# Optimization experiments

Hardware: AMD Instinct MI355X
Metric: run time of the kernel (lower is better)

Reference implementation:

```python
import jax, jax.numpy as jnp
import numpy as np
import math

ROPE_THETA = 10000.0


def apply_rope(x, positions):
    # x: [B, H, S, d_k], positions: [S]
    d_k = x.shape[-1]
    inv_freq = 1.0 / (ROPE_THETA ** (jnp.arange(0, d_k, 2, dtype=jnp.float32) / d_k))  # [d_k/2]
    angles = positions.astype(jnp.float32)[:, None] * inv_freq[None, :]  # [S, d_k/2]
    cos = jnp.cos(angles)
    sin = jnp.sin(angles)
    x1 = x[..., 0::2]
    x2 = x[..., 1::2]
    r1 = x1 * cos - x2 * sin
    r2 = x1 * sin + x2 * cos
    out = jnp.stack([r1, r2], axis=-1)  # interleave pairs back
    return out.reshape(x.shape)


def setup_inputs() -> dict:
    key = jax.random.key(0)
    k1, k2, k3 = jax.random.split(key, 3)
    B, S, D = 4, 2048, 1024
    x = jax.random.normal(k1, (B, S, D), dtype=jnp.float32)
    token_positions = jnp.arange(S, dtype=jnp.int32)
    w_qkv = jax.random.normal(k2, (3 * D, D), dtype=jnp.float32) * (1.0 / math.sqrt(D))
    w_o = jax.random.normal(k3, (D, D), dtype=jnp.float32) * (1.0 / math.sqrt(D))
    return {"x": x, "token_positions": token_positions, "w_qkv": w_qkv, "w_o": w_o}


def reference(x, token_positions, w_qkv, w_o):
    B, S, D = x.shape
    H = 16
    d_k = D // H
    qkv = jnp.einsum('bsd,ed->bse', x, w_qkv)  # [B, S, 3D]
    # rearrange '... s (stack h dk) -> stack ... h s dk'
    qkv = qkv.reshape(B, S, 3, H, d_k)
    q = jnp.transpose(qkv[:, :, 0], (0, 2, 1, 3))  # [B, H, S, dk]
    k = jnp.transpose(qkv[:, :, 1], (0, 2, 1, 3))
    v = jnp.transpose(qkv[:, :, 2], (0, 2, 1, 3))
    q = apply_rope(q, token_positions)
    k = apply_rope(k, token_positions)
    scores = jnp.einsum('bhqd,bhkd->bhqk', q, k) / math.sqrt(d_k)
    causal = jnp.tril(jnp.ones((S, S), dtype=bool))
    scores = jnp.where(causal[None, None], scores, -jnp.inf)
    attn = jax.nn.softmax(scores, axis=-1)
    out = jnp.einsum('bhqk,bhkd->bhqd', attn, v)  # [B, H, S, dk]
    out = jnp.transpose(out, (0, 2, 1, 3)).reshape(B, S, D)
    return jnp.einsum('bsd,ed->bse', out, w_o)
```

## Files before the change

kernel.cpp:

```cpp
#include <hip/hip_runtime.h>
#include <hip/hip_bf16.h>
#include <math.h>

typedef __bf16 bf16_t;
typedef __attribute__((ext_vector_type(8))) __bf16 bf16x8;
typedef __attribute__((ext_vector_type(4))) __bf16 bf16x4;
typedef __attribute__((ext_vector_type(4))) float f32x4;

#define MFMA_16x16x32(A_, B_, C_) __builtin_amdgcn_mfma_f32_16x16x32_bf16((A_), (B_), (C_), 0, 0, 0)

#define Bsz 4
#define Ssz 2048
#define Dsz 1024
#define Hh 16
#define DKd 64
#define Mrows (Bsz * Ssz)
#define N1 (3 * Dsz)
#define KD Dsz

__global__ void cvt_f32_bf16_kernel(const float* __restrict__ src, bf16_t* __restrict__ dst, int n4) {
  int i = blockIdx.x * blockDim.x + threadIdx.x;
  if (i >= n4) return;
  float4 v = reinterpret_cast<const float4*>(src)[i];
  bf16x4 o = {(bf16_t)v.x, (bf16_t)v.y, (bf16_t)v.z, (bf16_t)v.w};
  reinterpret_cast<bf16x4*>(dst)[i] = o;
}

__global__ void rope_tab_kernel(const int* __restrict__ pos, float2* __restrict__ tab) {
  int i = blockIdx.x * blockDim.x + threadIdx.x;
  if (i >= Ssz * 32) return;
  int s = i >> 5, f = i & 31;
  float inv_freq = powf(10000.0f, -(float)(2 * f) / 64.0f);
  float a = (float)pos[s] * inv_freq;
  tab[i] = make_float2(cosf(a), sinf(a));
}

template <int EPI>
__global__ __launch_bounds__(256, 3) void gemm_tn_kernel(
    const bf16_t* __restrict__ A, const bf16_t* __restrict__ Bt, int Kdim, int ldcN,
    bf16_t* __restrict__ qb, bf16_t* __restrict__ kb, bf16_t* __restrict__ vtb,
    const float2* __restrict__ tab, float* __restrict__ fout) {
  __shared__ __align__(16) bf16_t As[2][128 * 32];
  __shared__ __align__(16) bf16_t Bs[2][128 * 32];
  const int t = threadIdx.x;
  const int w = t >> 6, l = t & 63;
  const int lr = l & 15, lk = l >> 4;
  const int wm = w >> 1, wn = w & 1;
  const int m0 = blockIdx.y * 128, n0 = blockIdx.x * 128;

  const int srow = t >> 2;
  const int schunk = (t & 3) ^ ((t >> 3) & 3);
  const bf16_t* gA = A + (size_t)(m0 + srow) * Kdim + schunk * 8;
  const bf16_t* gB = Bt + (size_t)(n0 + srow) * Kdim + schunk * 8;

  f32x4 acc[4][4] = {};
  const int rsw = (lr >> 1) & 3;

#define STAGE_(PH, KT)                                                                   \
  do {                                                                                   \
    __builtin_amdgcn_global_load_lds(gA + (KT), &As[PH][(w * 16) * 32], 16, 0, 0);       \
    __builtin_amdgcn_global_load_lds(gA + (size_t)64 * Kdim + (KT),                      \
                                     &As[PH][(64 + w * 16) * 32], 16, 0, 0);             \
    __builtin_amdgcn_global_load_lds(gB + (KT), &Bs[PH][(w * 16) * 32], 16, 0, 0);       \
    __builtin_amdgcn_global_load_lds(gB + (size_t)64 * Kdim + (KT),                      \
                                     &Bs[PH][(64 + w * 16) * 32], 16, 0, 0);             \
  } while (0)

#define COMPUTE_(PH)                                                                     \
  do {                                                                                   \
    bf16x8 af[4], bfv[4];                                                                \
    _Pragma("unroll") for (int m = 0; m < 4; ++m) af[m] =                                \
        *reinterpret_cast<const bf16x8*>(&As[PH][(wm * 64 + m * 16 + lr) * 32] +         \
                                         ((lk ^ rsw) * 8));                              \
    _Pragma("unroll") for (int n = 0; n < 4; ++n) bfv[n] =                               \
        *reinterpret_cast<const bf16x8*>(&Bs[PH][(wn * 64 + n * 16 + lr) * 32] +         \
                                         ((lk ^ rsw) * 8));                              \
    _Pragma("unroll") for (int m = 0; m < 4; ++m) _Pragma("unroll") for (int n = 0;      \
                                                                         n < 4; ++n)    \
        acc[m][n] = MFMA_16x16x32(af[m], bfv[n], acc[m][n]);                             \
  } while (0)

  STAGE_(0, 0);
  __syncthreads();
  for (int kt = 0; kt < Kdim; kt += 64) {
    STAGE_(1, kt + 32);
    COMPUTE_(0);
    __syncthreads();
    if (kt + 64 < Kdim) STAGE_(0, kt + 64);
    COMPUTE_(1);
    __syncthreads();
  }
#undef STAGE_
#undef COMPUTE_

  if (EPI == 0) {
#pragma unroll
    for (int n = 0; n < 4; ++n) {
      const int col = n0 + wn * 64 + n * 16 + lr;
      const int sect = col >> 10;
      const int h = (col >> 6) & 15;
      const int dk = col & 63;
#pragma unroll
      for (int m = 0; m < 4; ++m) {
        const int growb = m0 + wm * 64 + m * 16 + lk * 4;
#pragma unroll
        for (int r = 0; r < 4; ++r) {
          const int grow = growb + r;
          const int bb = grow >> 11;
          const int s = grow & (Ssz - 1);
          float v = acc[m][n][r];
          if (sect < 2) {
            const float pv = __shfl_xor(v, 1);
            const float2 cs = tab[(s << 5) | (dk >> 1)];
            float vr = (dk & 1) ? (pv * cs.y + v * cs.x) : (v * cs.x - pv * cs.y);
            const size_t idx = ((size_t)((bb * Hh + h) * Ssz + s)) * DKd + dk;
            if (sect == 0)
              qb[idx] = (bf16_t)(vr * 0.125f);
            else
              kb[idx] = (bf16_t)vr;
          } else {
            vtb[((size_t)(bb * Hh + h) * DKd + dk) * Ssz + s] = (bf16_t)v;
          }
        }
      }
    }
  } else {
#pragma unroll
    for (int m = 0; m < 4; ++m)
#pragma unroll
      for (int r = 0; r < 4; ++r) {
        const int grow = m0 + wm * 64 + m * 16 + lk * 4 + r;
        float* op = fout + (size_t)grow * ldcN + n0 + wn * 64 + lr;
#pragma unroll
        for (int n = 0; n < 4; ++n) op[n * 16] = acc[m][n][r];
      }
  }
}

__global__ __launch_bounds__(256, 3) void attn_kernel(
    const bf16_t* __restrict__ qb, const bf16_t* __restrict__ kb,
    const bf16_t* __restrict__ vtb, bf16_t* __restrict__ aout) {
  __shared__ __align__(16) bf16_t Ks[64 * 64];
  __shared__ __align__(16) bf16_t Vs[64 * 64];
  const int t = threadIdx.x, w = t >> 6, l = t & 63;
  const int lr = l & 15, lk = l >> 4;
  const int bid = blockIdx.x;
  const int bh = (bid & 7) * 8 + ((bid >> 3) & 7);
  const int qt = 15 - (bid >> 6);
  const int q0 = qt * 128;
  const int sub0 = q0 + w * 32;

  const bf16_t* qbase = qb + ((size_t)bh * Ssz + sub0) * DKd;
  bf16x8 qf[2][2];
#pragma unroll
  for (int s = 0; s < 2; ++s) {
    qf[s][0] = *reinterpret_cast<const bf16x8*>(qbase + (s * 16 + lr) * DKd + lk * 8);
    qf[s][1] = *reinterpret_cast<const bf16x8*>(qbase + (s * 16 + lr) * DKd + 32 + lk * 8);
  }

  f32x4 o[2][4] = {};
  float mrow[2] = {-INFINITY, -INFINITY};
  float lsum[2] = {0.f, 0.f};

  const int srow = t >> 2;
  const int scc = (t & 3) * 2;
  const bf16_t* kg = kb + ((size_t)bh * Ssz + srow) * DKd + scc * 8;
  const bf16_t* vg = vtb + ((size_t)bh * DKd + srow) * Ssz + scc * 8;
  bf16_t* ksw0 = Ks + srow * 64 + ((scc ^ (srow & 7)) * 8);
  bf16_t* ksw1 = Ks + srow * 64 + (((scc + 1) ^ (srow & 7)) * 8);
  bf16_t* vw[4];
#pragma unroll
  for (int u = 0; u < 2; ++u) {
    const int c = scc + u;
    const int B = 32 * (c >> 2) + 16 * (c & 1) + 4 * ((c & 3) >> 1);
    const int ch = B >> 3, off = B & 7;
    vw[2 * u] = Vs + srow * 64 + ((ch ^ (srow & 7)) * 8) + off;
    vw[2 * u + 1] = Vs + srow * 64 + (((ch + 1) ^ (srow & 7)) * 8) + off;
  }

  const int kvend = q0 + 128;
  bf16x8 pk0 = *reinterpret_cast<const bf16x8*>(kg);
  bf16x8 pk1 = *reinterpret_cast<const bf16x8*>(kg + 8);
  bf16x8 pv0 = *reinterpret_cast<const bf16x8*>(vg);
  bf16x8 pv1 = *reinterpret_cast<const bf16x8*>(vg + 8);

  for (int kv = 0; kv < kvend; kv += 64) {
    __syncthreads();
    *reinterpret_cast<bf16x8*>(ksw0) = pk0;
    *reinterpret_cast<bf16x8*>(ksw1) = pk1;
    *reinterpret_cast<bf16x4*>(vw[0]) = __builtin_shufflevector(pv0, pv0, 0, 1, 2, 3);
    *reinterpret_cast<bf16x4*>(vw[1]) = __builtin_shufflevector(pv0, pv0, 4, 5, 6, 7);
    *reinterpret_cast<bf16x4*>(vw[2]) = __builtin_shufflevector(pv1, pv1, 0, 1, 2, 3);
    *reinterpret_cast<bf16x4*>(vw[3]) = __builtin_shufflevector(pv1, pv1, 4, 5, 6, 7);
    __syncthreads();
    if (kv + 64 < kvend) {
      pk0 = *reinterpret_cast<const bf16x8*>(kg + (size_t)(kv + 64) * DKd);
      pk1 = *reinterpret_cast<const bf16x8*>(kg + (size_t)(kv + 64) * DKd + 8);
      pv0 = *reinterpret_cast<const bf16x8*>(vg + kv + 64);
      pv1 = *reinterpret_cast<const bf16x8*>(vg + kv + 64 + 8);
    }
#pragma unroll
    for (int s = 0; s < 2; ++s) {
      const int subrow = sub0 + s * 16;
      if (kv > subrow + 15) continue;
      f32x4 sa[4];
#pragma unroll
      for (int n = 0; n < 4; ++n) {
        const int R = n * 16 + lr;
        const bf16x8 a0 = *reinterpret_cast<const bf16x8*>(Ks + R * 64 + ((lk ^ (R & 7)) * 8));
        const bf16x8 a1 = *reinterpret_cast<const bf16x8*>(Ks + R * 64 + (((lk + 4) ^ (R & 7)) * 8));
        f32x4 z = {};
        z = MFMA_16x16x32(a0, qf[s][0], z);
        z = MFMA_16x16x32(a1, qf[s][1], z);
        sa[n] = z;
      }
      if (kv + 63 > subrow) {
        const int qrow = subrow + lr;
        const int kbase = kv + lk * 4;
#pragma unroll
        for (int n = 0; n < 4; ++n)
#pragma unroll
          for (int r = 0; r < 4; ++r)
            if (kbase + n * 16 + r > qrow) sa[n][r] = -INFINITY;
      }
      float mx = fmaxf(fmaxf(fmaxf(sa[0][0], sa[0][1]), fmaxf(sa[0][2], sa[0][3])),
                       fmaxf(fmaxf(sa[1][0], sa[1][1]), fmaxf(sa[1][2], sa[1][3])));
      mx = fmaxf(mx, fmaxf(fmaxf(fmaxf(sa[2][0], sa[2][1]), fmaxf(sa[2][2], sa[2][3])),
                           fmaxf(fmaxf(sa[3][0], sa[3][1]), fmaxf(sa[3][2], sa[3][3]))));
      mx = fmaxf(mx, __shfl_xor(mx, 16));
      mx = fmaxf(mx, __shfl_xor(mx, 32));
      const float mnew = fmaxf(mrow[s], mx);
      const float scl = __expf(mrow[s] - mnew);
      mrow[s] = mnew;
      float ps = 0.f;
#pragma unroll
      for (int n = 0; n < 4; ++n)
#pragma unroll
        for (int r = 0; r < 4; ++r) {
          const float p = __expf(sa[n][r] - mnew);
          sa[n][r] = p;
          ps += p;
        }
      lsum[s] = lsum[s] * scl + ps;
#pragma unroll
      for (int n = 0; n < 4; ++n)
#pragma unroll
        for (int r = 0; r < 4; ++r) o[s][n][r] *= scl;
      bf16x8 pb0, pb1;
#pragma unroll
      for (int r = 0; r < 4; ++r) {
        pb0[r] = (bf16_t)sa[0][r];
        pb0[4 + r] = (bf16_t)sa[1][r];
        pb1[r] = (bf16_t)sa[2][r];
        pb1[4 + r] = (bf16_t)sa[3][r];
      }
#pragma unroll
      for (int n = 0; n < 4; ++n) {
        const int R = n * 16 + lr;
        const bf16x8 v0 = *reinterpret_cast<const bf16x8*>(Vs + R * 64 + ((lk ^ (R & 7)) * 8));
        const bf16x8 v1 = *reinterpret_cast<const bf16x8*>(Vs + R * 64 + (((lk + 4) ^ (R & 7)) * 8));
        o[s][n] = MFMA_16x16x32(v0, pb0, o[s][n]);
        o[s][n] = MFMA_16x16x32(v1, pb1, o[s][n]);
      }
    }
  }
  const int b_ = bh >> 4, h_ = bh & 15;
#pragma unroll
  for (int s = 0; s < 2; ++s) {
    float sm = lsum[s];
    sm += __shfl_xor(sm, 16);
    sm += __shfl_xor(sm, 32);
    const float inv = 1.0f / sm;
    const int qrow = sub0 + s * 16 + lr;
    bf16_t* op = aout + ((size_t)b_ * Ssz + qrow) * Dsz + h_ * DKd + lk * 4;
#pragma unroll
    for (int n = 0; n < 4; ++n) {
      const bf16x4 ov = {(bf16_t)(o[s][n][0] * inv), (bf16_t)(o[s][n][1] * inv),
                         (bf16_t)(o[s][n][2] * inv), (bf16_t)(o[s][n][3] * inv)};
      *reinterpret_cast<bf16x4*>(op + n * 16) = ov;
    }
  }
}

extern "C" void kernel_launch(void* const* d_in, const int* in_sizes, int n_in,
                              void* d_out, int out_size, void* d_ws, size_t ws_size,
                              hipStream_t stream) {
  const float* x = (const float*)d_in[0];
  const int* pos = (const int*)d_in[1];
  const float* wqkv = (const float*)d_in[2];
  const float* wo = (const float*)d_in[3];
  float* out = (float*)d_out;

  bf16_t* xb = (bf16_t*)d_ws;
  bf16_t* wqkvb = xb + (size_t)Mrows * KD;
  bf16_t* wob = wqkvb + (size_t)N1 * KD;
  bf16_t* qbuf = wob + (size_t)Dsz * KD;
  bf16_t* kbuf = qbuf + (size_t)64 * Ssz * DKd;
  bf16_t* vtb = kbuf + (size_t)64 * Ssz * DKd;
  float2* tab = (float2*)(vtb + (size_t)64 * Ssz * DKd);
  bf16_t* aout = xb;

  {
    int n4 = Mrows * KD / 4;
    cvt_f32_bf16_kernel<<<(n4 + 255) / 256, 256, 0, stream>>>(x, xb, n4);
  }
  {
    int n4 = N1 * KD / 4;
    cvt_f32_bf16_kernel<<<(n4 + 255) / 256, 256, 0, stream>>>(wqkv, wqkvb, n4);
  }
  {
    int n4 = Dsz * KD / 4;
    cvt_f32_bf16_kernel<<<(n4 + 255) / 256, 256, 0, stream>>>(wo, wob, n4);
  }
  rope_tab_kernel<<<(Ssz * 32 + 255) / 256, 256, 0, stream>>>(pos, tab);

  gemm_tn_kernel<0><<<dim3(N1 / 128, Mrows / 128), 256, 0, stream>>>(
      xb, wqkvb, KD, 0, qbuf, kbuf, vtb, tab, nullptr);

  attn_kernel<<<dim3(16 * 64), 256, 0, stream>>>(qbuf, kbuf, vtb, aout);

  gemm_tn_kernel<1><<<dim3(Dsz / 128, Mrows / 128), 256, 0, stream>>>(
      aout, wob, KD, Dsz, nullptr, nullptr, nullptr, nullptr, out);
}
```

Baseline: 217.8 us.

## Add 256x256-tile QKV GEMM with direct global-to-LDS loads

```diff
diff --git a/kernel.cpp b/kernel.cpp
--- a/kernel.cpp
+++ b/kernel.cpp
@@ -35,11 +35,119 @@
   tab[i] = make_float2(cosf(a), sinf(a));
 }
 
-template <int EPI>
-__global__ __launch_bounds__(256, 3) void gemm_tn_kernel(
+__global__ __launch_bounds__(512, 2) void gemm256_qkv_kernel(
+    const bf16_t* __restrict__ A, const bf16_t* __restrict__ Bt,
+    bf16_t* __restrict__ qb, bf16_t* __restrict__ kb, bf16_t* __restrict__ vtb,
+    const float2* __restrict__ tab) {
+  __shared__ __align__(16) bf16_t As[2][256 * 64];
+  __shared__ __align__(16) bf16_t Bs[2][256 * 64];
+  const int t = threadIdx.x;
+  const int w = t >> 6, l = t & 63;
+  const int lr = l & 15, lk = l >> 4;
+  const int rs = lr >> 1;
+  const int wm = w >> 2, wn = w & 3;
+  const int m0 = blockIdx.y * 256, n0 = blockIdx.x * 256;
+
+  const int trow = t >> 3;
+  const int schunk = (t & 7) ^ ((t >> 4) & 7);
+  const bf16_t* gAs[4];
+  const bf16_t* gBs[4];
+#pragma unroll
+  for (int i = 0; i < 4; ++i) {
+    gAs[i] = A + (size_t)(m0 + i * 64 + trow) * KD + schunk * 8;
+    gBs[i] = Bt + (size_t)(n0 + i * 64 + trow) * KD + schunk * 8;
+  }
+
+  f32x4 acc[8][4] = {};
+
+#pragma unroll
+  for (int i = 0; i < 4; ++i) {
+    __builtin_amdgcn_global_load_lds(gAs[i], &As[0][(i * 64 + w * 8) * 64], 16, 0, 0);
+    __builtin_amdgcn_global_load_lds(gBs[i], &Bs[0][(i * 64 + w * 8) * 64], 16, 0, 0);
+  }
+  __syncthreads();
+
+  for (int tt = 0; tt < KD / 64; ++tt) {
+    const int b = tt & 1;
+    if (tt + 1 < KD / 64) {
+      const int kt = (tt + 1) * 64;
+#pragma unroll
+      for (int i = 0; i < 4; ++i) {
+        __builtin_amdgcn_global_load_lds(gAs[i] + kt, &As[b ^ 1][(i * 64 + w * 8) * 64], 16, 0, 0);
+        __builtin_amdgcn_global_load_lds(gBs[i] + kt, &Bs[b ^ 1][(i * 64 + w * 8) * 64], 16, 0, 0);
+      }
+    }
+    bf16x8 bfv[4][2];
+#pragma unroll
+    for (int n = 0; n < 4; ++n) {
+      const int R = wn * 64 + n * 16 + lr;
+#pragma unroll
+      for (int ks = 0; ks < 2; ++ks)
+        bfv[n][ks] = *reinterpret_cast<const bf16x8*>(&Bs[b][R * 64 + (((ks * 4 + lk) ^ rs) * 8)]);
+    }
+#pragma unroll
+    for (int mp = 0; mp < 4; ++mp) {
+      bf16x8 af[2][2];
+#pragma unroll
+      for (int mi = 0; mi < 2; ++mi) {
+        const int R = wm * 128 + (mp * 2 + mi) * 16 + lr;
+#pragma unroll
+        for (int ks = 0; ks < 2; ++ks)
+          af[mi][ks] = *reinterpret_cast<const bf16x8*>(&As[b][R * 64 + (((ks * 4 + lk) ^ rs) * 8)]);
+      }
+      __builtin_amdgcn_s_setprio(1);
+#pragma unroll
+      for (int mi = 0; mi < 2; ++mi)
+#pragma unroll
+        for (int n = 0; n < 4; ++n) {
+          acc[mp * 2 + mi][n] = MFMA_16x16x32(af[mi][0], bfv[n][0], acc[mp * 2 + mi][n]);
+          acc[mp * 2 + mi][n] = MFMA_16x16x32(af[mi][1], bfv[n][1], acc[mp * 2 + mi][n]);
+        }
+      __builtin_amdgcn_s_setprio(0);
+    }
+    __syncthreads();
+  }
+
+  const int sect = n0 >> 10;
+  const int hh = ((n0 + wn * 64) >> 6) & 15;
+  if (sect < 2) {
+#pragma unroll
+    for (int m = 0; m < 8; ++m)
+#pragma unroll
+      for (int r = 0; r < 4; ++r) {
+        const int grow = m0 + wm * 128 + m * 16 + lk * 4 + r;
+        const int bb = grow >> 11, s = grow & (Ssz - 1);
+        const float2* tr = tab + (s << 5);
+        bf16_t* basep = (sect == 0 ? qb : kb) + ((size_t)(bb * Hh + hh) * Ssz + s) * DKd;
+#pragma unroll
+        for (int n = 0; n < 4; ++n) {
+          const float v = acc[m][n][r];
+          const float pv = __shfl_xor(v, 1);
+          const int dk = n * 16 + lr;
+          const float2 cs = tr[dk >> 1];
+          float vr = (dk & 1) ? (pv * cs.y + v * cs.x) : (v * cs.x - pv * cs.y);
+          if (sect == 0) vr *= 0.125f;
+          basep[dk] = (bf16_t)vr;
+        }
+      }
+  } else {
+#pragma unroll
+    for (int m = 0; m < 8; ++m)
+#pragma unroll
+      for (int r = 0; r < 4; ++r) {
+        const int grow = m0 + wm * 128 + m * 16 + lk * 4 + r;
+        const int bb = grow >> 11, s = grow & (Ssz - 1);
+        bf16_t* vb = vtb + (size_t)(bb * Hh + hh) * DKd * Ssz + s;
+#pragma unroll
+        for (int n = 0; n < 4; ++n)
+          vb[(size_t)(n * 16 + lr) * Ssz] = (bf16_t)acc[m][n][r];
+      }
+  }
+}
+
+__global__ __launch_bounds__(256, 3) void gemm_out_kernel(
     const bf16_t* __restrict__ A, const bf16_t* __restrict__ Bt, int Kdim, int ldcN,
-    bf16_t* __restrict__ qb, bf16_t* __restrict__ kb, bf16_t* __restrict__ vtb,
-    const float2* __restrict__ tab, float* __restrict__ fout) {
+    float* __restrict__ fout) {
   __shared__ __align__(16) bf16_t As[2][128 * 32];
   __shared__ __align__(16) bf16_t Bs[2][128 * 32];
   const int t = threadIdx.x;
@@ -93,48 +201,15 @@
 #undef STAGE_
 #undef COMPUTE_
 
-  if (EPI == 0) {
-#pragma unroll
-    for (int n = 0; n < 4; ++n) {
-      const int col = n0 + wn * 64 + n * 16 + lr;
-      const int sect = col >> 10;
-      const int h = (col >> 6) & 15;
-      const int dk = col & 63;
-#pragma unroll
-      for (int m = 0; m < 4; ++m) {
-        const int growb = m0 + wm * 64 + m * 16 + lk * 4;
-#pragma unroll
-        for (int r = 0; r < 4; ++r) {
-          const int grow = growb + r;
-          const int bb = grow >> 11;
-          const int s = grow & (Ssz - 1);
-          float v = acc[m][n][r];
-          if (sect < 2) {
-            const float pv = __shfl_xor(v, 1);
-            const float2 cs = tab[(s << 5) | (dk >> 1)];
-            float vr = (dk & 1) ? (pv * cs.y + v * cs.x) : (v * cs.x - pv * cs.y);
-            const size_t idx = ((size_t)((bb * Hh + h) * Ssz + s)) * DKd + dk;
-            if (sect == 0)
-              qb[idx] = (bf16_t)(vr * 0.125f);
-            else
-              kb[idx] = (bf16_t)vr;
-          } else {
-            vtb[((size_t)(bb * Hh + h) * DKd + dk) * Ssz + s] = (bf16_t)v;
-          }
-        }
-      }
-    }
-  } else {
-#pragma unroll
-    for (int m = 0; m < 4; ++m)
-#pragma unroll
-      for (int r = 0; r < 4; ++r) {
-        const int grow = m0 + wm * 64 + m * 16 + lk * 4 + r;
-        float* op = fout + (size_t)grow * ldcN + n0 + wn * 64 + lr;
-#pragma unroll
-        for (int n = 0; n < 4; ++n) op[n * 16] = acc[m][n][r];
-      }
-  }
+#pragma unroll
+  for (int m = 0; m < 4; ++m)
+#pragma unroll
+    for (int r = 0; r < 4; ++r) {
+      const int grow = m0 + wm * 64 + m * 16 + lk * 4 + r;
+      float* op = fout + (size_t)grow * ldcN + n0 + wn * 64 + lr;
+#pragma unroll
+      for (int n = 0; n < 4; ++n) op[n * 16] = acc[m][n][r];
+    }
 }
 
 __global__ __launch_bounds__(256, 3) void attn_kernel(
@@ -314,11 +389,11 @@
   }
   rope_tab_kernel<<<(Ssz * 32 + 255) / 256, 256, 0, stream>>>(pos, tab);
 
-  gemm_tn_kernel<0><<<dim3(N1 / 128, Mrows / 128), 256, 0, stream>>>(
-      xb, wqkvb, KD, 0, qbuf, kbuf, vtb, tab, nullptr);
+  gemm256_qkv_kernel<<<dim3(N1 / 256, Mrows / 256), 512, 0, stream>>>(
+      xb, wqkvb, qbuf, kbuf, vtb, tab);
 
   attn_kernel<<<dim3(16 * 64), 256, 0, stream>>>(qbuf, kbuf, vtb, aout);
 
-  gemm_tn_kernel<1><<<dim3(Dsz / 128, Mrows / 128), 256, 0, stream>>>(
-      aout, wob, KD, Dsz, nullptr, nullptr, nullptr, nullptr, out);
-}
+  gemm_out_kernel<<<dim3(Dsz / 128, Mrows / 128), 256, 0, stream>>>(
+      aout, wob, KD, Dsz, out);
+}
```

Result: faster. 197.9 us (-9.1%).
